# Performance work log

Hardware: AMD Instinct MI355X
Metric: run time of the kernel (lower is better)

Reference implementation:

```python
import jax, jax.numpy as jnp
import numpy as np

B, S, H, NH = 2, 2048, 2048, 16
DH = H // NH


def setup_inputs() -> dict:
    key = jax.random.key(0)
    ks = jax.random.split(key, 9)
    scale = 1.0 / np.sqrt(H)
    inp = {
        "hidden_state": jax.random.normal(ks[0], (B, S, H), dtype=jnp.float32),
        "Wq": jax.random.normal(ks[1], (H, H), dtype=jnp.float32) * scale,
        "bq": jnp.zeros((H,), dtype=jnp.float32),
        "Wk": jax.random.normal(ks[2], (H, H), dtype=jnp.float32) * scale,
        "bk": jnp.zeros((H,), dtype=jnp.float32),
        "Wv": jax.random.normal(ks[3], (H, H), dtype=jnp.float32) * scale,
        "bv": jnp.zeros((H,), dtype=jnp.float32),
        "Wo": jax.random.normal(ks[4], (H, H), dtype=jnp.float32) * scale,
        "bo": jnp.zeros((H,), dtype=jnp.float32),
    }
    # additive causal mask: 0 on/below diagonal, large negative above
    neg = jnp.float32(-1e9)
    tri = jnp.tril(jnp.ones((S, S), dtype=bool))
    inp["causal_mask"] = jnp.where(tri, 0.0, neg)[None, None, :, :]
    return inp


def reference(hidden_state, Wq, bq, Wk, bk, Wv, bv, Wo, bo, causal_mask):
    def split_heads(x):  # [B,S,H] -> [B,NH,S,DH]
        return x.reshape(B, S, NH, DH).transpose(0, 2, 1, 3)

    q = split_heads(hidden_state @ Wq + bq)
    k = split_heads(hidden_state @ Wk + bk)
    v = split_heads(hidden_state @ Wv + bv)

    scores = jnp.einsum("bhqd,bhkd->bhqk", q, k) / jnp.sqrt(jnp.float32(DH))
    scores = scores + causal_mask
    probs = jax.nn.softmax(scores, axis=-1)
    out = jnp.einsum("bhqk,bhkd->bhqd", probs, v)  # [B,NH,S,DH]
    out = out.transpose(0, 2, 1, 3).reshape(B, S, H)
    return out @ Wo + bo
```

## Files before the change

### kernel.cpp

```cpp
#include <hip/hip_runtime.h>
#include <cstdint>

typedef __attribute__((ext_vector_type(4))) float f32x4;
typedef __attribute__((ext_vector_type(16))) float f32x16;
typedef __attribute__((ext_vector_type(8))) __bf16 bf16x8;
typedef __attribute__((ext_vector_type(4))) unsigned short u16x4;
typedef __attribute__((ext_vector_type(2))) unsigned int u32x2;
typedef __attribute__((ext_vector_type(4))) float fvec4;

#define DEV __device__ __forceinline__
#define MFMA16(a, b, c) __builtin_amdgcn_mfma_f32_16x16x32_bf16((a), (b), (c), 0, 0, 0)
#define MFMA32(a, b, c) __builtin_amdgcn_mfma_f32_32x32x16_bf16((a), (b), (c), 0, 0, 0)

DEV unsigned short f2bf(float f) {
  union { float f; uint32_t u; } c; c.f = f;
  uint32_t u = c.u;
  return (unsigned short)((u + 0x7FFFu + ((u >> 16) & 1u)) >> 16);
}

DEV unsigned int pack2(float lo, float hi) {
  union { float f; uint32_t u; } a, b;
  a.f = lo; b.f = hi;
  return __builtin_amdgcn_perm(b.u + 0x8000u, a.u + 0x8000u, 0x07060302u);
}

DEV void gll16(const void* g, void* l) {
  __builtin_amdgcn_global_load_lds(
      (const __attribute__((address_space(1))) void*)(uintptr_t)g,
      (__attribute__((address_space(3))) void*)(uint32_t)(uintptr_t)l,
      16, 0, 0);
}

__global__ void cvt_bf16(const float* __restrict__ src, unsigned short* __restrict__ dst) {
  int i = (blockIdx.x * 256 + threadIdx.x) * 4;
  fvec4 v = *(const fvec4*)(src + i);
  u16x4 o;
  o[0] = f2bf(v[0]); o[1] = f2bf(v[1]); o[2] = f2bf(v[2]); o[3] = f2bf(v[3]);
  *(u16x4*)(dst + i) = o;
}

__global__ void transpose_cvt4(const float* __restrict__ W0, const float* __restrict__ W1,
                               const float* __restrict__ W2, const float* __restrict__ W3,
                               unsigned short* __restrict__ Dqkv, unsigned short* __restrict__ Do) {
  __shared__ float t[32][33];
  const float* W = blockIdx.z == 0 ? W0 : blockIdx.z == 1 ? W1 : blockIdx.z == 2 ? W2 : W3;
  unsigned short* WT = blockIdx.z < 3 ? Dqkv + (size_t)blockIdx.z * 2048 * 2048 : Do;
  int n0 = blockIdx.x * 32, k0 = blockIdx.y * 32;
  int x = threadIdx.x, y = threadIdx.y;
  #pragma unroll
  for (int i = 0; i < 32; i += 8)
    t[y + i][x] = W[(size_t)(k0 + y + i) * 2048 + n0 + x];
  __syncthreads();
  #pragma unroll
  for (int i = 0; i < 32; i += 8)
    WT[(size_t)(n0 + y + i) * 2048 + k0 + x] = f2bf(t[x][y + i]);
}

constexpr float QSC = 0.08838834764831845f * 1.4426950408889634f;

template <int MODE>
__global__ __launch_bounds__(256, 2) void gemm128(
    const unsigned short* __restrict__ A,
    const unsigned short* __restrict__ Bt,
    const float* __restrict__ b0, const float* __restrict__ b1,
    const float* __restrict__ b2,
    void* __restrict__ o0, void* __restrict__ o1, void* __restrict__ o2) {
  __shared__ unsigned short As[128 * 64];
  __shared__ unsigned short Bs[128 * 64];
  const int id = blockIdx.x;
  const int m0 = (((id & 7) << 2) | ((id >> 3) & 3)) * 128;
  const int n0 = (id >> 5) * 128;
  const int tid = threadIdx.x;
  const int wave = tid >> 6, lid = tid & 63;
  const int l16 = lid & 15, lq = lid >> 4;
  const int wm = (wave >> 1) * 64, wn = (wave & 1) * 64;

  const int srow = lid >> 3;
  const int sgrp = (lid & 7) ^ srow;

  f32x4 acc[4][4] = {};

  for (int k0 = 0; k0 < 2048; k0 += 64) {
    #pragma unroll
    for (int i = 0; i < 4; ++i) {
      const int t = wave * 4 + i;
      const int r = t * 8 + srow;
      gll16(A + (size_t)(m0 + r) * 2048 + k0 + sgrp * 8, (char*)As + t * 1024 + lid * 16);
      gll16(Bt + (size_t)(n0 + r) * 2048 + k0 + sgrp * 8, (char*)Bs + t * 1024 + lid * 16);
    }
    __syncthreads();
    #pragma unroll
    for (int kk = 0; kk < 2; ++kk) {
      const int G = kk * 4 + lq;
      bf16x8 af[4], bfr[4];
      #pragma unroll
      for (int i = 0; i < 4; ++i)
        af[i] = *(const bf16x8*)(As + (wm + i * 16 + l16) * 64 + ((G ^ (l16 & 7)) << 3));
      #pragma unroll
      for (int j = 0; j < 4; ++j)
        bfr[j] = *(const bf16x8*)(Bs + (wn + j * 16 + l16) * 64 + ((G ^ (l16 & 7)) << 3));
      #pragma unroll
      for (int i = 0; i < 4; ++i)
        #pragma unroll
        for (int j = 0; j < 4; ++j)
          acc[i][j] = MFMA16(af[i], bfr[j], acc[i][j]);
    }
    __syncthreads();
  }

  #pragma unroll
  for (int j = 0; j < 4; ++j) {
    const int c = n0 + wn + j * 16 + l16;
    const float bv = b0[c];
    #pragma unroll
    for (int i = 0; i < 4; ++i)
      #pragma unroll
      for (int r = 0; r < 4; ++r) {
        const int row = m0 + wm + i * 16 + lq * 4 + r;
        ((float*)o0)[(size_t)row * 2048 + c] = acc[i][j][r] + bv;
      }
  }
}

__global__ __launch_bounds__(512, 2) void gemmqkv(
    const unsigned short* __restrict__ A,
    const unsigned short* __restrict__ Bt,
    const float* __restrict__ b0, const float* __restrict__ b1,
    const float* __restrict__ b2,
    unsigned short* __restrict__ oQ, unsigned short* __restrict__ oK,
    unsigned short* __restrict__ oV) {
  __shared__ unsigned short Als[2 * 256 * 64];
  __shared__ unsigned short Bls[2 * 192 * 64];

  const int id = blockIdx.x;
  const int xcd = id & 7, loc = id >> 3;
  const int nt = xcd * 4 + (loc >> 4);
  const int mt = loc & 15;
  const int m0 = mt << 8, n0 = nt * 192;

  const int tid = threadIdx.x;
  const int wave = tid >> 6, lid = tid & 63;
  const int l16 = lid & 15, lq = lid >> 4;
  const int wr = wave >> 2, wc = wave & 3;
  const int srow = tid >> 3;
  const int g8 = ((tid & 7) ^ (srow & 7)) * 8;

  f32x4 acc[8][3] = {};
  bf16x8 aq[8][2], bq[3][2];

#define STA_(c, kt) do { \
    _Pragma("unroll") for (int u = 0; u < 4; ++u) \
      gll16(A + (size_t)(m0 + u * 64 + srow) * 2048 + ((kt) << 6) + g8, \
            (char*)Als + (c) * 32768 + u * 8192 + tid * 16); \
  } while (0)

#define STB_(c, kt) do { \
    _Pragma("unroll") for (int u = 0; u < 3; ++u) \
      gll16(Bt + (size_t)(n0 + u * 64 + srow) * 2048 + ((kt) << 6) + g8, \
            (char*)Bls + (c) * 24576 + u * 8192 + tid * 16); \
  } while (0)

#define RDALL_(c) do { \
    _Pragma("unroll") for (int mf = 0; mf < 8; ++mf) { \
      const int row = wr * 128 + mf * 16 + l16; \
      _Pragma("unroll") for (int kk = 0; kk < 2; ++kk) \
        aq[mf][kk] = *(const bf16x8*)(Als + (c) * 16384 + row * 64 + \
                                      (((kk * 4 + lq) ^ (row & 7)) << 3)); \
    } \
    _Pragma("unroll") for (int n = 0; n < 3; ++n) { \
      const int bg = wc * 48 + n * 16 + l16; \
      _Pragma("unroll") for (int kk = 0; kk < 2; ++kk) \
        bq[n][kk] = *(const bf16x8*)(Bls + (c) * 12288 + bg * 64 + \
                                     (((kk * 4 + lq) ^ (bg & 7)) << 3)); \
    } } while (0)

#define MM_(h) do { \
    _Pragma("unroll") for (int m = 0; m < 4; ++m) \
      _Pragma("unroll") for (int n = 0; n < 3; ++n) \
        _Pragma("unroll") for (int kk = 0; kk < 2; ++kk) \
          acc[(h) * 4 + m][n] = MFMA16(aq[(h) * 4 + m][kk], bq[n][kk], acc[(h) * 4 + m][n]); \
  } while (0)

#define SB_ __builtin_amdgcn_sched_barrier(0)
#define BAR_ __builtin_amdgcn_s_barrier()
#define LGKM_ asm volatile("s_waitcnt lgkmcnt(0)" ::: "memory")
#define VM7_ asm volatile("s_waitcnt vmcnt(7)" ::: "memory")

  STA_(0, 0); STB_(0, 0);
  STA_(1, 1); STB_(1, 1);
  VM7_;
  BAR_;

  #pragma unroll 1
  for (int t = 0; t < 32; ++t) {
    const int c = t & 1;
    const int tn = (t + 2 < 32) ? t + 2 : 31;
    RDALL_(c);
    SB_; LGKM_; SB_;
    __builtin_amdgcn_s_setprio(1); MM_(0); __builtin_amdgcn_s_setprio(0);
    SB_; BAR_;
    STA_(c, tn); STB_(c, tn);
    SB_;
    __builtin_amdgcn_s_setprio(1); MM_(1); __builtin_amdgcn_s_setprio(0);
    SB_; VM7_;
    BAR_;
  }
  asm volatile("s_waitcnt vmcnt(0)" ::: "memory");

  #pragma unroll
  for (int n = 0; n < 3; ++n) {
    const int cgl = n0 + wc * 48 + n * 16 + l16;
    const int which = cgl >> 11;
    const int hd = cgl & 2047;
    const int h = hd >> 7, d = hd & 127;
    const float* bp = which == 0 ? b0 : which == 1 ? b1 : b2;
    const float bv = bp[hd];
    if (which == 2) {
      #pragma unroll
      for (int m = 0; m < 8; ++m) {
        const int row0 = m0 + wr * 128 + m * 16 + lq * 4;
        const int bb = row0 >> 11, s0 = row0 & 2047;
        u16x4 pv;
        #pragma unroll
        for (int r = 0; r < 4; ++r) pv[r] = f2bf(acc[m][n][r] + bv);
        *(u16x4*)(oV + ((size_t)((bb * 16 + h) * 128 + d)) * 2048 + s0) = pv;
      }
    } else {
      const float sc = which == 0 ? QSC : 1.0f;
      unsigned short* op = which == 0 ? oQ : oK;
      #pragma unroll
      for (int m = 0; m < 8; ++m)
        #pragma unroll
        for (int r = 0; r < 4; ++r) {
          const int row = m0 + wr * 128 + m * 16 + lq * 4 + r;
          const int bb = row >> 11, s = row & 2047;
          op[(size_t)((bb * 16 + h) * 2048 + s) * 128 + d] = f2bf((acc[m][n][r] + bv) * sc);
        }
    }
  }
#undef STA_
#undef STB_
#undef RDALL_
#undef MM_
#undef SB_
#undef BAR_
#undef LGKM_
#undef VM7_
}

__global__ __launch_bounds__(256, 2) void attn(
    const unsigned short* __restrict__ Q,
    const unsigned short* __restrict__ K,
    const unsigned short* __restrict__ Vt,
    unsigned short* __restrict__ ctx) {
  __shared__ unsigned short Ks[64 * 128];
  __shared__ unsigned short Vts[128 * 64];
  __shared__ unsigned short Ps[4 * 32 * 64];

  const int bh = blockIdx.y;
  const int jq = (bh < 16) ? (15 - (int)blockIdx.x) : (int)blockIdx.x;
  const int q0 = jq * 128;
  const int b = bh >> 4, h = bh & 15;
  const unsigned short* Qh = Q + (size_t)bh * 2048 * 128;
  const unsigned short* Kh = K + (size_t)bh * 2048 * 128;
  const unsigned short* Vth = Vt + (size_t)bh * 128 * 2048;

  const int tid = threadIdx.x;
  const int wave = tid >> 6, lid = tid & 63;
  const int l32 = lid & 31, half = lid >> 5;
  const int qrow = q0 + wave * 32 + l32;
  unsigned short* Pw = Ps + wave * 2048 + l32 * 64;
  const int qsw = l32 & 7;

  bf16x8 qf[8];
  #pragma unroll
  for (int ds = 0; ds < 8; ++ds)
    qf[ds] = *(const bf16x8*)(Qh + (size_t)qrow * 128 + ds * 16 + half * 8);

  float m_i = -1e30f, l_i = 0.f;
  f32x16 acc[4] = {};

  const int ntiles = 2 * jq + 2;
  for (int jt = 0; jt < ntiles; ++jt) {
    const int k0 = jt * 64;
    #pragma unroll
    for (int ii = 0; ii < 4; ++ii) {
      const int t = wave * 4 + ii;
      const int r = t * 4 + (lid >> 4);
      const int g = (lid & 15) ^ (r & 15);
      gll16(Kh + (size_t)(k0 + r) * 128 + g * 8, (char*)Ks + t * 1024 + lid * 16);
    }
    #pragma unroll
    for (int ii = 0; ii < 4; ++ii) {
      const int t = wave * 4 + ii;
      const int d = t * 8 + (lid >> 3);
      const int g = (lid & 7) ^ (d & 7);
      gll16(Vth + (size_t)d * 2048 + k0 + g * 8, (char*)Vts + t * 1024 + lid * 16);
    }
    __syncthreads();

    f32x16 sacc[2] = {};
    #pragma unroll
    for (int ds = 0; ds < 8; ++ds) {
      #pragma unroll
      for (int mb = 0; mb < 2; ++mb) {
        const int kr = mb * 32 + l32;
        bf16x8 af = *(const bf16x8*)(Ks + kr * 128 + (((ds * 2 + half) ^ (kr & 15)) << 3));
        sacc[mb] = MFMA32(af, qf[ds], sacc[mb]);
      }
    }

    if (jt >= 2 * jq) {
      #pragma unroll
      for (int mb = 0; mb < 2; ++mb)
        #pragma unroll
        for (int i = 0; i < 16; ++i) {
          const int kg = k0 + mb * 32 + (i & 3) + 8 * (i >> 2) + 4 * half;
          if (kg > qrow) sacc[mb][i] = -1e30f;
        }
    }

    float tmax = -1e30f;
    #pragma unroll
    for (int mb = 0; mb < 2; ++mb)
      #pragma unroll
      for (int i = 0; i < 16; ++i) tmax = fmaxf(tmax, sacc[mb][i]);
    tmax = fmaxf(tmax, __shfl_xor(tmax, 32));

    const float mnew = fmaxf(m_i, tmax);
    const float alpha = exp2f(m_i - mnew);
    m_i = mnew;

    float ps = 0.f;
    #pragma unroll
    for (int mb = 0; mb < 2; ++mb) {
      #pragma unroll
      for (int i = 0; i < 16; ++i) {
        sacc[mb][i] = exp2f(sacc[mb][i] - mnew);
        ps += sacc[mb][i];
      }
      #pragma unroll
      for (int u = 0; u < 4; ++u) {
        u32x2 w;
        w[0] = pack2(sacc[mb][4 * u], sacc[mb][4 * u + 1]);
        w[1] = pack2(sacc[mb][4 * u + 2], sacc[mb][4 * u + 3]);
        *(u32x2*)(Pw + (((u + mb * 4) ^ qsw) << 3) + half * 4) = w;
      }
    }
    ps += __shfl_xor(ps, 32);
    l_i = l_i * alpha + ps;
    #pragma unroll
    for (int db = 0; db < 4; ++db)
      #pragma unroll
      for (int i = 0; i < 16; ++i) acc[db][i] *= alpha;

    #pragma unroll
    for (int ks = 0; ks < 4; ++ks) {
      bf16x8 pf = *(const bf16x8*)(Pw + (((ks * 2 + half) ^ qsw) << 3));
      #pragma unroll
      for (int db = 0; db < 4; ++db) {
        const int d = db * 32 + l32;
        bf16x8 vf = *(const bf16x8*)(Vts + d * 64 + (((ks * 2 + half) ^ (d & 7)) << 3));
        acc[db] = MFMA32(vf, pf, acc[db]);
      }
    }
    __syncthreads();
  }

  const float inv = 1.f / l_i;
  const size_t base = ((size_t)(b * 2048 + qrow)) * 2048 + h * 128;
  #pragma unroll
  for (int db = 0; db < 4; ++db) {
    #pragma unroll
    for (int u = 0; u < 4; ++u) {
      u32x2 w;
      w[0] = pack2(acc[db][4 * u] * inv, acc[db][4 * u + 1] * inv);
      w[1] = pack2(acc[db][4 * u + 2] * inv, acc[db][4 * u + 3] * inv);
      *(u32x2*)(ctx + base + db * 32 + 8 * u + 4 * half) = w;
    }
  }
}

extern "C" void kernel_launch(void* const* d_in, const int* in_sizes, int n_in,
                              void* d_out, int out_size, void* d_ws, size_t ws_size,
                              hipStream_t stream) {
  const float* hs = (const float*)d_in[0];
  const float* Wq = (const float*)d_in[1];
  const float* bq = (const float*)d_in[2];
  const float* Wk = (const float*)d_in[3];
  const float* bk = (const float*)d_in[4];
  const float* Wv = (const float*)d_in[5];
  const float* bv = (const float*)d_in[6];
  const float* Wo = (const float*)d_in[7];
  const float* bo = (const float*)d_in[8];
  float* out = (float*)d_out;

  char* ws = (char*)d_ws;
  unsigned short* hsb   = (unsigned short*)(ws);
  unsigned short* wqkvt = (unsigned short*)(ws + (16 << 20));
  unsigned short* wot   = (unsigned short*)(ws + (40 << 20));
  unsigned short* Qb    = (unsigned short*)(ws + (48 << 20));
  unsigned short* Kb    = (unsigned short*)(ws + (64 << 20));
  unsigned short* Vtb   = (unsigned short*)(ws + (80 << 20));
  unsigned short* ctx   = (unsigned short*)(ws + (96 << 20));

  cvt_bf16<<<dim3(8192), dim3(256), 0, stream>>>(hs, hsb);
  transpose_cvt4<<<dim3(64, 64, 4), dim3(32, 8), 0, stream>>>(Wq, Wk, Wv, Wo, wqkvt, wot);

  gemmqkv<<<dim3(512), dim3(512), 0, stream>>>(hsb, wqkvt, bq, bk, bv, Qb, Kb, Vtb);
  attn<<<dim3(16, 32), 256, 0, stream>>>(Qb, Kb, Vtb, ctx);
  gemm128<0><<<dim3(512), 256, 0, stream>>>(ctx, wot, bo, nullptr, nullptr,
                                            (void*)out, nullptr, nullptr);
}
```

Baseline: 388.6 us.

## Remap QKV GEMM waves to 4x2 grid and interleave LDS reads with MFMA

Reassigns the 8 waves in the QKV projection GEMM from a 2x4 layout (128x48 per wave) to a 4x2 layout (64x96 per wave), changing the A/B fragment mix each wave reads from LDS. The first half of the MFMA work is no longer behind an lgkmcnt(0) wait. Those fragment reads can now be scheduled alongside the first MFMAs. Per-wave LDS traffic falls (4x2 A plus 6x2 B fragments instead of 8x2 plus 3x2), but the first half loses its priority boost and may have to wait on LDS reads anyway.

```diff
diff --git a/kernel.cpp b/kernel.cpp
--- a/kernel.cpp
+++ b/kernel.cpp
@@ -141,12 +141,12 @@
   const int tid = threadIdx.x;
   const int wave = tid >> 6, lid = tid & 63;
   const int l16 = lid & 15, lq = lid >> 4;
-  const int wr = wave >> 2, wc = wave & 3;
+  const int wr = wave >> 1, wc2 = wave & 1;
   const int srow = tid >> 3;
   const int g8 = ((tid & 7) ^ (srow & 7)) * 8;
 
-  f32x4 acc[8][3] = {};
-  bf16x8 aq[8][2], bq[3][2];
+  f32x4 acc[4][6] = {};
+  bf16x8 aq[4][2], bq[6][2];
 
 #define STA_(c, kt) do { \
     _Pragma("unroll") for (int u = 0; u < 4; ++u) \
@@ -160,25 +160,27 @@
             (char*)Bls + (c) * 24576 + u * 8192 + tid * 16); \
   } while (0)
 
-#define RDALL_(c) do { \
-    _Pragma("unroll") for (int mf = 0; mf < 8; ++mf) { \
-      const int row = wr * 128 + mf * 16 + l16; \
-      _Pragma("unroll") for (int kk = 0; kk < 2; ++kk) \
-        aq[mf][kk] = *(const bf16x8*)(Als + (c) * 16384 + row * 64 + \
-                                      (((kk * 4 + lq) ^ (row & 7)) << 3)); \
-    } \
-    _Pragma("unroll") for (int n = 0; n < 3; ++n) { \
-      const int bg = wc * 48 + n * 16 + l16; \
+#define RDB_(c) do { \
+    _Pragma("unroll") for (int n = 0; n < 6; ++n) { \
+      const int bg = wc2 * 96 + n * 16 + l16; \
       _Pragma("unroll") for (int kk = 0; kk < 2; ++kk) \
         bq[n][kk] = *(const bf16x8*)(Bls + (c) * 12288 + bg * 64 + \
                                      (((kk * 4 + lq) ^ (bg & 7)) << 3)); \
     } } while (0)
 
-#define MM_(h) do { \
-    _Pragma("unroll") for (int m = 0; m < 4; ++m) \
-      _Pragma("unroll") for (int n = 0; n < 3; ++n) \
+#define RDA_(c) do { \
+    _Pragma("unroll") for (int m = 0; m < 4; ++m) { \
+      const int row = wr * 64 + m * 16 + l16; \
+      _Pragma("unroll") for (int kk = 0; kk < 2; ++kk) \
+        aq[m][kk] = *(const bf16x8*)(Als + (c) * 16384 + row * 64 + \
+                                     (((kk * 4 + lq) ^ (row & 7)) << 3)); \
+    } } while (0)
+
+#define MMH_(h) do { \
+    _Pragma("unroll") for (int m = (h) * 2; m < (h) * 2 + 2; ++m) \
+      _Pragma("unroll") for (int n = 0; n < 6; ++n) \
         _Pragma("unroll") for (int kk = 0; kk < 2; ++kk) \
-          acc[(h) * 4 + m][n] = MFMA16(aq[(h) * 4 + m][kk], bq[n][kk], acc[(h) * 4 + m][n]); \
+          acc[m][n] = MFMA16(aq[m][kk], bq[n][kk], acc[m][n]); \
   } while (0)
 
 #define SB_ __builtin_amdgcn_sched_barrier(0)
@@ -195,21 +197,21 @@
   for (int t = 0; t < 32; ++t) {
     const int c = t & 1;
     const int tn = (t + 2 < 32) ? t + 2 : 31;
-    RDALL_(c);
-    SB_; LGKM_; SB_;
-    __builtin_amdgcn_s_setprio(1); MM_(0); __builtin_amdgcn_s_setprio(0);
-    SB_; BAR_;
+    SB_;
+    RDB_(c); RDA_(c);
+    MMH_(0);
+    LGKM_; SB_; BAR_;
     STA_(c, tn); STB_(c, tn);
     SB_;
-    __builtin_amdgcn_s_setprio(1); MM_(1); __builtin_amdgcn_s_setprio(0);
+    __builtin_amdgcn_s_setprio(1); MMH_(1); __builtin_amdgcn_s_setprio(0);
     SB_; VM7_;
     BAR_;
   }
   asm volatile("s_waitcnt vmcnt(0)" ::: "memory");
 
   #pragma unroll
-  for (int n = 0; n < 3; ++n) {
-    const int cgl = n0 + wc * 48 + n * 16 + l16;
+  for (int n = 0; n < 6; ++n) {
+    const int cgl = n0 + wc2 * 96 + n * 16 + l16;
     const int which = cgl >> 11;
     const int hd = cgl & 2047;
     const int h = hd >> 7, d = hd & 127;
@@ -217,8 +219,8 @@
     const float bv = bp[hd];
     if (which == 2) {
       #pragma unroll
-      for (int m = 0; m < 8; ++m) {
-        const int row0 = m0 + wr * 128 + m * 16 + lq * 4;
+      for (int m = 0; m < 4; ++m) {
+        const int row0 = m0 + wr * 64 + m * 16 + lq * 4;
         const int bb = row0 >> 11, s0 = row0 & 2047;
         u16x4 pv;
         #pragma unroll
@@ -229,10 +231,10 @@
       const float sc = which == 0 ? QSC : 1.0f;
       unsigned short* op = which == 0 ? oQ : oK;
       #pragma unroll
-      for (int m = 0; m < 8; ++m)
+      for (int m = 0; m < 4; ++m)
         #pragma unroll
         for (int r = 0; r < 4; ++r) {
-          const int row = m0 + wr * 128 + m * 16 + lq * 4 + r;
+          const int row = m0 + wr * 64 + m * 16 + lq * 4 + r;
           const int bb = row >> 11, s = row & 2047;
           op[(size_t)((bb * 16 + h) * 2048 + s) * 128 + d] = f2bf((acc[m][n][r] + bv) * sc);
         }
@@ -240,8 +242,9 @@
   }
 #undef STA_
 #undef STB_
-#undef RDALL_
-#undef MM_
+#undef RDB_
+#undef RDA_
+#undef MMH_
 #undef SB_
 #undef BAR_
 #undef LGKM_
```

New measurement: 382.0 us. About the same (-1.7%).
